# Performance work log

Measured on AMD Instinct MI355X. Metric: run time of the kernel, lower is better.

Reference implementation:

```python
import jax, jax.numpy as jnp
import numpy as np

C = 256
CI = C // 2  # inter_channel = 128
B, H, W = 8, 64, 64


def setup_inputs() -> dict:
    key = jax.random.key(0)
    ks = jax.random.split(key, 9)
    s = 0.02
    return {
        "x": jax.random.normal(ks[0], (B, C, H, W), jnp.float32),
        "w_phi": jax.random.normal(ks[1], (CI, C), jnp.float32) * s,
        "b_phi": jax.random.normal(ks[2], (CI,), jnp.float32) * s,
        "w_theta": jax.random.normal(ks[3], (CI, C), jnp.float32) * s,
        "b_theta": jax.random.normal(ks[4], (CI,), jnp.float32) * s,
        "w_g": jax.random.normal(ks[5], (CI, C), jnp.float32) * s,
        "b_g": jax.random.normal(ks[6], (CI,), jnp.float32) * s,
        "w_mask": jax.random.normal(ks[7], (C, CI), jnp.float32) * s,
        "b_mask": jax.random.normal(ks[8], (C,), jnp.float32) * s,
    }


def reference(x, w_phi, b_phi, w_theta, b_theta, w_g, b_g, w_mask, b_mask):
    b, c, h, w = x.shape
    n = h * w
    xf = x.reshape(b, c, n)  # [b, c, n]
    # 1x1 convs == per-position channel projections
    phi = jnp.einsum('dc,bcn->bdn', w_phi, xf) + b_phi[:, None]      # [b, ci, n]
    theta = jnp.einsum('dc,bcn->bnd', w_theta, xf) + b_theta[None, None, :]  # [b, n, ci]
    g = jnp.einsum('dc,bcn->bnd', w_g, xf) + b_g[None, None, :]      # [b, n, ci]
    # full self-attention over spatial positions (no scaling, as in source)
    scores = jnp.einsum('bnd,bdm->bnm', theta, phi)                  # [b, n, n]
    attn = jax.nn.softmax(scores, axis=-1)
    y = jnp.einsum('bnm,bmd->bnd', attn, g)                          # [b, n, ci]
    # mask conv (1x1) back to channel dim + residual
    mask = jnp.einsum('cd,bnd->bcn', w_mask, y) + b_mask[:, None]    # [b, c, n]
    return mask.reshape(b, c, h, w) + x
```

## Files before the change

### kernel.cpp

```cpp
#include <hip/hip_runtime.h>

#define BB 8
#define CC 256
#define DD 128
#define NN 4096

#define LOG2E 1.44269504f
#define MSHIFT 32.0f

typedef __attribute__((ext_vector_type(8))) short short8;
typedef __attribute__((ext_vector_type(4))) short short4v;
typedef __attribute__((ext_vector_type(4))) float f32x4;

static __device__ __forceinline__ unsigned short f2bf(float f) {
    unsigned u = __builtin_bit_cast(unsigned, f);
    u += 0x7FFFu + ((u >> 16) & 1u);
    return (unsigned short)(u >> 16);
}
static __device__ __forceinline__ unsigned short f2bf_trunc(float f) {
    return (unsigned short)(__builtin_bit_cast(unsigned, f) >> 16);
}
static __device__ __forceinline__ float bf2f(unsigned short h) {
    unsigned u = ((unsigned)h) << 16;
    return __builtin_bit_cast(float, u);
}
static __device__ __forceinline__ short8 pack8(float4 a, float4 b) {
    short8 r;
    r[0] = (short)f2bf(a.x); r[1] = (short)f2bf(a.y);
    r[2] = (short)f2bf(a.z); r[3] = (short)f2bf(a.w);
    r[4] = (short)f2bf(b.x); r[5] = (short)f2bf(b.y);
    r[6] = (short)f2bf(b.z); r[7] = (short)f2bf(b.w);
    return r;
}

__global__ __launch_bounds__(256) void k_transpose_x(
        const float* __restrict__ x, unsigned short* __restrict__ xT) {
    __shared__ __align__(16) unsigned short tile[64][66];
    int nb = blockIdx.x * 64, cb = blockIdx.y * 64, b = blockIdx.z;
    const float* xp = x + (size_t)b * CC * NN;
    int t = threadIdx.x;
#pragma unroll
    for (int i = 0; i < 2; i++) {
        int idx = t + 256 * i;
        int c_l = idx >> 3;
        int n0 = (idx & 7) * 8;
        const float* src = xp + (size_t)(cb + c_l) * NN + nb + n0;
        float4 v0 = *(const float4*)(src);
        float4 v1 = *(const float4*)(src + 4);
        tile[n0 + 0][c_l] = f2bf(v0.x);
        tile[n0 + 1][c_l] = f2bf(v0.y);
        tile[n0 + 2][c_l] = f2bf(v0.z);
        tile[n0 + 3][c_l] = f2bf(v0.w);
        tile[n0 + 4][c_l] = f2bf(v1.x);
        tile[n0 + 5][c_l] = f2bf(v1.y);
        tile[n0 + 6][c_l] = f2bf(v1.z);
        tile[n0 + 7][c_l] = f2bf(v1.w);
    }
    __syncthreads();
    unsigned short* xtp = xT + (size_t)b * NN * CC;
#pragma unroll
    for (int i = 0; i < 2; i++) {
        int idx = t + 256 * i;
        int n_l = idx >> 3;
        int c0 = (idx & 7) * 8;
        const unsigned int* row = (const unsigned int*)&tile[n_l][0];
        uint4 o;
        o.x = row[(c0 >> 1) + 0];
        o.y = row[(c0 >> 1) + 1];
        o.z = row[(c0 >> 1) + 2];
        o.w = row[(c0 >> 1) + 3];
        *(uint4*)(xtp + (size_t)(nb + n_l) * CC + cb + c0) = o;
    }
}

__global__ __launch_bounds__(256) void k_proj(
        const unsigned short* __restrict__ xT,
        const float* __restrict__ w_phi, const float* __restrict__ b_phi,
        const float* __restrict__ w_theta, const float* __restrict__ b_theta,
        const float* __restrict__ w_g, const float* __restrict__ b_g,
        unsigned short* __restrict__ qws, unsigned short* __restrict__ kws,
        unsigned short* __restrict__ vtws) {
    __shared__ __align__(16) unsigned short xs[128][72];
    __shared__ __align__(16) unsigned short rp[128][136];
    int nb = blockIdx.x * 128, proj = blockIdx.y, b = blockIdx.z;
    const float *W, *bias;
    if (proj == 0) { W = w_theta; bias = b_theta; }
    else if (proj == 1) { W = w_phi; bias = b_phi; }
    else { W = w_g; bias = b_g; }
    float scl = (proj == 0) ? LOG2E : 1.0f;
    int t = threadIdx.x, lane = t & 63, wave = t >> 6;
    int l16 = lane & 15, l4 = lane >> 4;

    f32x4 acc[2][8];
#pragma unroll
    for (int mf = 0; mf < 2; mf++)
#pragma unroll
        for (int nf = 0; nf < 8; nf++)
#pragma unroll
            for (int e = 0; e < 4; e++) acc[mf][nf][e] = 0.f;

    const unsigned short* xtp = xT + (size_t)b * NN * CC;
    for (int kc = 0; kc < 4; kc++) {
        int c0k = kc * 64;
        __syncthreads();
#pragma unroll
        for (int i = 0; i < 4; i++) {
            int idx = t + 256 * i;
            int n = idx >> 3, cc = (idx & 7) * 8;
            *(short8*)&xs[n][cc] = *(const short8*)(xtp + (size_t)(nb + n) * CC + c0k + cc);
        }
        __syncthreads();
        short8 af[2][2];
#pragma unroll
        for (int mf = 0; mf < 2; mf++)
#pragma unroll
            for (int ic = 0; ic < 2; ic++) {
                int d = wave * 32 + mf * 16 + l16;
                const float* wp = W + d * CC + c0k + ic * 32 + l4 * 8;
                af[mf][ic] = pack8(*(const float4*)wp, *(const float4*)(wp + 4));
            }
#pragma unroll
        for (int nf = 0; nf < 8; nf++)
#pragma unroll
            for (int ic = 0; ic < 2; ic++) {
                short8 bfr = *(const short8*)&xs[nf * 16 + l16][ic * 32 + l4 * 8];
                acc[0][nf] = __builtin_amdgcn_mfma_f32_16x16x32_bf16(af[0][ic], bfr, acc[0][nf], 0, 0, 0);
                acc[1][nf] = __builtin_amdgcn_mfma_f32_16x16x32_bf16(af[1][ic], bfr, acc[1][nf], 0, 0, 0);
            }
    }
    __syncthreads();
    if (proj < 2) {
        unsigned short* outp = (proj == 0 ? qws : kws) + (size_t)b * NN * DD;
#pragma unroll
        for (int mf = 0; mf < 2; mf++) {
            int d0 = wave * 32 + mf * 16 + l4 * 4;
            float bb[4];
#pragma unroll
            for (int r = 0; r < 4; r++) bb[r] = bias[d0 + r];
#pragma unroll
            for (int nf = 0; nf < 8; nf++) {
                short4v pk;
#pragma unroll
                for (int r = 0; r < 4; r++) pk[r] = (short)f2bf((acc[mf][nf][r] + bb[r]) * scl);
                *(short4v*)&rp[nf * 16 + l16][d0] = pk;
            }
        }
        __syncthreads();
#pragma unroll
        for (int i = 0; i < 8; i++) {
            int idx = t + 256 * i;
            int n = idx >> 4, dd = (idx & 15) * 8;
            *(short8*)(outp + (size_t)(nb + n) * DD + dd) = *(const short8*)&rp[n][dd];
        }
    } else {
#pragma unroll
        for (int mf = 0; mf < 2; mf++) {
            int drow = wave * 32 + mf * 16 + l4 * 4;
            float bb[4];
#pragma unroll
            for (int r = 0; r < 4; r++) bb[r] = bias[drow + r];
#pragma unroll
            for (int nf = 0; nf < 8; nf++)
#pragma unroll
                for (int r = 0; r < 4; r++)
                    rp[drow + r][nf * 16 + l16] = f2bf(acc[mf][nf][r] + bb[r]);
        }
        __syncthreads();
        unsigned short* outp = vtws + (size_t)b * DD * NN;
#pragma unroll
        for (int i = 0; i < 8; i++) {
            int idx = t + 256 * i;
            int d = idx >> 4, n0 = (idx & 15) * 8;
            *(short8*)(outp + (size_t)d * NN + nb + n0) = *(const short8*)&rp[d][n0];
        }
    }
}

__global__ __launch_bounds__(128, 4) void k_flash(
        const unsigned short* __restrict__ q, const unsigned short* __restrict__ kk,
        const unsigned short* __restrict__ vt, unsigned short* __restrict__ opart,
        float* __restrict__ lsums) {
    __shared__ __align__(16) unsigned short smem[12032];
    unsigned short (*Kt)[136] = (unsigned short (*)[136])smem;
    unsigned short (*Vt)[40]  = (unsigned short (*)[40])(smem + 4352);
    unsigned short (*Pt)[32][40] = (unsigned short (*)[32][40])(smem + 9472);

    int qb = blockIdx.x * 64, ks = blockIdx.y, b = blockIdx.z;
    int t = threadIdx.x, lane = t & 63, wave = t >> 6;
    int l16 = lane & 15, l4 = lane >> 4;
    const unsigned short* qp = q + (size_t)b * NN * DD;
    const unsigned short* kp = kk + (size_t)b * NN * DD;
    const unsigned short* vp = vt + (size_t)b * DD * NN;

    short8 qf[2][4];
#pragma unroll
    for (int m = 0; m < 2; m++) {
        int qrow = qb + wave * 32 + m * 16 + l16;
#pragma unroll
        for (int kc = 0; kc < 4; kc++)
            qf[m][kc] = *(const short8*)(qp + (size_t)qrow * DD + kc * 32 + l4 * 8);
    }

    f32x4 o[2][8];
    float lsum[2][4];
#pragma unroll
    for (int m = 0; m < 2; m++) {
#pragma unroll
        for (int df = 0; df < 8; df++)
#pragma unroll
            for (int e = 0; e < 4; e++) o[m][df][e] = 0.f;
#pragma unroll
        for (int r = 0; r < 4; r++) lsum[m][r] = 0.f;
    }

    int kbase = ks * (NN / 2);
    for (int it = 0; it < (NN / 2) / 32; ++it) {
        int mb = kbase + it * 32;
        __syncthreads();
#pragma unroll
        for (int i = 0; i < 4; i++) {
            int idx = t + 128 * i;
            int mr = idx >> 4, d0 = (idx & 15) * 8;
            *(short8*)&Kt[mr][d0] = *(const short8*)(kp + (size_t)(mb + mr) * DD + d0);
        }
#pragma unroll
        for (int i = 0; i < 4; i++) {
            int idx = t + 128 * i;
            int dr = idx >> 2, m0 = (idx & 3) * 8;
            *(short8*)&Vt[dr][m0] = *(const short8*)(vp + (size_t)dr * NN + mb + m0);
        }
        __syncthreads();

        f32x4 s[2][2];
#pragma unroll
        for (int m = 0; m < 2; m++)
#pragma unroll
            for (int nf = 0; nf < 2; nf++)
#pragma unroll
                for (int e = 0; e < 4; e++) s[m][nf][e] = -MSHIFT;
#pragma unroll
        for (int kc = 0; kc < 4; kc++)
#pragma unroll
            for (int nf = 0; nf < 2; nf++) {
                short8 bfr = *(const short8*)&Kt[nf * 16 + l16][kc * 32 + l4 * 8];
                s[0][nf] = __builtin_amdgcn_mfma_f32_16x16x32_bf16(qf[0][kc], bfr, s[0][nf], 0, 0, 0);
                s[1][nf] = __builtin_amdgcn_mfma_f32_16x16x32_bf16(qf[1][kc], bfr, s[1][nf], 0, 0, 0);
            }

#pragma unroll
        for (int m = 0; m < 2; m++)
#pragma unroll
            for (int nf = 0; nf < 2; nf++)
#pragma unroll
                for (int r = 0; r < 4; r++) {
                    float p = __builtin_exp2f(s[m][nf][r]);
                    lsum[m][r] += p;
                    Pt[wave][m * 16 + l4 * 4 + r][nf * 16 + l16] = f2bf_trunc(p);
                }
        asm volatile("s_waitcnt lgkmcnt(0)" ::: "memory");

        short8 pa0 = *(const short8*)&Pt[wave][l16][l4 * 8];
        short8 pa1 = *(const short8*)&Pt[wave][16 + l16][l4 * 8];
#pragma unroll
        for (int df = 0; df < 8; df++) {
            short8 vb = *(const short8*)&Vt[df * 16 + l16][l4 * 8];
            o[0][df] = __builtin_amdgcn_mfma_f32_16x16x32_bf16(pa0, vb, o[0][df], 0, 0, 0);
            o[1][df] = __builtin_amdgcn_mfma_f32_16x16x32_bf16(pa1, vb, o[1][df], 0, 0, 0);
        }
    }

    __syncthreads();
    unsigned short (*Ox)[136] = (unsigned short (*)[136])smem;
    float* Ls = (float*)((char*)smem + 17408);
    int rb = wave * 32;
#pragma unroll
    for (int m = 0; m < 2; m++) {
#pragma unroll
        for (int df = 0; df < 8; df++)
#pragma unroll
            for (int r = 0; r < 4; r++)
                Ox[rb + m * 16 + l4 * 4 + r][df * 16 + l16] = f2bf(o[m][df][r]);
#pragma unroll
        for (int r = 0; r < 4; r++) {
            float v = lsum[m][r];
            v += __shfl_xor(v, 1);
            v += __shfl_xor(v, 2);
            v += __shfl_xor(v, 4);
            v += __shfl_xor(v, 8);
            if (l16 == 0) Ls[rb + m * 16 + l4 * 4 + r] = v;
        }
    }
    __syncthreads();
    unsigned short* op = opart + (((size_t)ks * BB + b) * NN + qb) * DD;
#pragma unroll
    for (int i = 0; i < 8; i++) {
        int idx = t + 128 * i;
        int nr = idx >> 4, d0 = (idx & 15) * 8;
        *(short8*)(op + (size_t)nr * DD + d0) = *(const short8*)&Ox[nr][d0];
    }
    if (t < 64) lsums[((size_t)ks * BB + b) * NN + qb + t] = Ls[t];
}

__global__ __launch_bounds__(256) void k_maskout(
        const unsigned short* __restrict__ opart, const float* __restrict__ lsums,
        const float* __restrict__ w_mask, const float* __restrict__ b_mask,
        const float* __restrict__ x, float* __restrict__ out) {
    __shared__ __align__(16) unsigned short Ys[64][136];
    __shared__ float invl[64];
    int nb = blockIdx.x * 64, cs = blockIdx.y, b = blockIdx.z;
    int t = threadIdx.x, lane = t & 63, wave = t >> 6;
    int l16 = lane & 15, l4 = lane >> 4;

    const unsigned short* o0 = opart + ((size_t)b * NN + nb) * DD;
    const unsigned short* o1 = opart + (((size_t)BB + b) * NN + nb) * DD;
    if (t < 64) {
        float ls0 = lsums[(size_t)b * NN + nb + t];
        float ls1 = lsums[((size_t)BB + b) * NN + nb + t];
        invl[t] = 1.0f / (ls0 + ls1);
    }
    __syncthreads();
#pragma unroll
    for (int i = 0; i < 4; i++) {
        int idx = t + 256 * i;
        int nr = idx >> 4, d0 = (idx & 15) * 8;
        short8 a = *(const short8*)(o0 + (size_t)nr * DD + d0);
        short8 c = *(const short8*)(o1 + (size_t)nr * DD + d0);
        float inv = invl[nr];
        short8 yv;
#pragma unroll
        for (int j = 0; j < 8; j++)
            yv[j] = (short)f2bf((bf2f((unsigned short)a[j]) + bf2f((unsigned short)c[j])) * inv);
        *(short8*)&Ys[nr][d0] = yv;
    }
    __syncthreads();

    f32x4 acc[2][4];
#pragma unroll
    for (int mf = 0; mf < 2; mf++)
#pragma unroll
        for (int nf = 0; nf < 4; nf++)
#pragma unroll
            for (int e = 0; e < 4; e++) acc[mf][nf][e] = 0.f;

#pragma unroll
    for (int kc = 0; kc < 4; kc++) {
        int d0 = kc * 32 + l4 * 8;
        short8 af[2];
#pragma unroll
        for (int mf = 0; mf < 2; mf++) {
            int c = cs * 128 + wave * 32 + mf * 16 + l16;
            const float* wp = w_mask + c * DD + d0;
            af[mf] = pack8(*(const float4*)wp, *(const float4*)(wp + 4));
        }
#pragma unroll
        for (int nf = 0; nf < 4; nf++) {
            short8 bfr = *(const short8*)&Ys[nf * 16 + l16][d0];
#pragma unroll
            for (int mf = 0; mf < 2; mf++)
                acc[mf][nf] = __builtin_amdgcn_mfma_f32_16x16x32_bf16(af[mf], bfr, acc[mf][nf], 0, 0, 0);
        }
    }

    const float* xp = x + (size_t)b * CC * NN;
    float* op = out + (size_t)b * CC * NN;
#pragma unroll
    for (int mf = 0; mf < 2; mf++) {
        int c0 = cs * 128 + wave * 32 + mf * 16 + l4 * 4;
        float bb[4];
#pragma unroll
        for (int r = 0; r < 4; r++) bb[r] = b_mask[c0 + r];
#pragma unroll
        for (int r = 0; r < 4; r++) {
            size_t rowoff = (size_t)(c0 + r) * NN;
#pragma unroll
            for (int nf = 0; nf < 4; nf++) {
                int n = nb + nf * 16 + l16;
                op[rowoff + n] = acc[mf][nf][r] + bb[r] + xp[rowoff + n];
            }
        }
    }
}

extern "C" void kernel_launch(void* const* d_in, const int* in_sizes, int n_in,
                              void* d_out, int out_size, void* d_ws, size_t ws_size,
                              hipStream_t stream) {
    const float* x       = (const float*)d_in[0];
    const float* w_phi   = (const float*)d_in[1];
    const float* b_phi   = (const float*)d_in[2];
    const float* w_theta = (const float*)d_in[3];
    const float* b_theta = (const float*)d_in[4];
    const float* w_g     = (const float*)d_in[5];
    const float* b_g     = (const float*)d_in[6];
    const float* w_mask  = (const float*)d_in[7];
    const float* b_mask  = (const float*)d_in[8];
    float* out = (float*)d_out;

    char* ws = (char*)d_ws;
    unsigned short* xT    = (unsigned short*)(ws);
    unsigned short* opart = (unsigned short*)(ws);
    unsigned short* qw    = (unsigned short*)(ws + ((size_t)16 << 20));
    unsigned short* kw    = (unsigned short*)(ws + ((size_t)24 << 20));
    unsigned short* vtw   = (unsigned short*)(ws + ((size_t)32 << 20));
    float*          lsums = (float*)(ws + ((size_t)40 << 20));

    k_transpose_x<<<dim3(NN / 64, CC / 64, BB), 256, 0, stream>>>(x, xT);
    k_proj<<<dim3(NN / 128, 3, BB), 256, 0, stream>>>(xT, w_phi, b_phi, w_theta, b_theta,
                                                      w_g, b_g, qw, kw, vtw);
    k_flash<<<dim3(NN / 64, 2, BB), 128, 0, stream>>>(qw, kw, vtw, opart, lsums);
    k_maskout<<<dim3(NN / 64, 2, BB), 256, 0, stream>>>(opart, lsums, w_mask, b_mask, x, out);
}
```

Baseline: 270.3 us.

## Restructure flash attention kernel with 32x32 MFMA, larger tiles and register prefetch

Rewrites the attention kernel so each 512-thread block handles 256 query rows with 64-key tiles. Scores are computed as K·Q^T using 32x32x16 bf16 MFMA, so the probability fragments can be turned into the next MFMA's A operand in registers via cvt_pk_bf16 and permlane32 swaps, removing the LDS round trip for P. K/V tiles are stored in XOR-swizzled shared memory, the next tile is prefetched into registers while the current one computes, and block IDs are remapped to spread batches across XCDs. In exchange, register pressure rises and shared memory per block grows, which may reduce occupancy.

```diff
diff --git a/kernel.cpp b/kernel.cpp
--- a/kernel.cpp
+++ b/kernel.cpp
@@ -11,14 +11,13 @@
 typedef __attribute__((ext_vector_type(8))) short short8;
 typedef __attribute__((ext_vector_type(4))) short short4v;
 typedef __attribute__((ext_vector_type(4))) float f32x4;
+typedef __attribute__((ext_vector_type(16))) float f32x16;
+typedef __attribute__((ext_vector_type(4))) unsigned int u32x4;
 
 static __device__ __forceinline__ unsigned short f2bf(float f) {
     unsigned u = __builtin_bit_cast(unsigned, f);
     u += 0x7FFFu + ((u >> 16) & 1u);
     return (unsigned short)(u >> 16);
-}
-static __device__ __forceinline__ unsigned short f2bf_trunc(float f) {
-    return (unsigned short)(__builtin_bit_cast(unsigned, f) >> 16);
 }
 static __device__ __forceinline__ float bf2f(unsigned short h) {
     unsigned u = ((unsigned)h) << 16;
@@ -31,6 +30,19 @@
     r[4] = (short)f2bf(b.x); r[5] = (short)f2bf(b.y);
     r[6] = (short)f2bf(b.z); r[7] = (short)f2bf(b.w);
     return r;
+}
+static __device__ __forceinline__ unsigned cvtpk_bf16(float lo, float hi) {
+    unsigned r;
+    asm("v_cvt_pk_bf16_f32 %0, %1, %2" : "=v"(r) : "v"(lo), "v"(hi));
+    return r;
+}
+static __device__ __forceinline__ void pl32swap(unsigned &a, unsigned &b) {
+#if __has_builtin(__builtin_amdgcn_permlane32_swap)
+    auto r = __builtin_amdgcn_permlane32_swap((int)a, (int)b, false, false);
+    a = (unsigned)r[0]; b = (unsigned)r[1];
+#else
+    asm("v_permlane32_swap_b32 %0, %1" : "+v"(a), "+v"(b));
+#endif
 }
 
 __global__ __launch_bounds__(256) void k_transpose_x(
@@ -176,129 +188,178 @@
     }
 }
 
-__global__ __launch_bounds__(128, 4) void k_flash(
+__global__ __launch_bounds__(512, 2) void k_flash(
         const unsigned short* __restrict__ q, const unsigned short* __restrict__ kk,
         const unsigned short* __restrict__ vt, unsigned short* __restrict__ opart,
         float* __restrict__ lsums) {
-    __shared__ __align__(16) unsigned short smem[12032];
-    unsigned short (*Kt)[136] = (unsigned short (*)[136])smem;
-    unsigned short (*Vt)[40]  = (unsigned short (*)[40])(smem + 4352);
-    unsigned short (*Pt)[32][40] = (unsigned short (*)[32][40])(smem + 9472);
-
-    int qb = blockIdx.x * 64, ks = blockIdx.y, b = blockIdx.z;
+    __shared__ __align__(16) unsigned char smem[49152];
+    unsigned short* Ksm = (unsigned short*)smem;
+    unsigned short* Vsm = (unsigned short*)(smem + 32768);
+
+    int bid = blockIdx.x + 16 * (blockIdx.y + 2 * blockIdx.z);
+    int lb = (bid & 7) * 32 + (bid >> 3);
+    int qt = lb & 15;
+    int ks = (lb >> 4) & 1;
+    int b  = lb >> 5;
+    int qb = qt * 256;
+
     int t = threadIdx.x, lane = t & 63, wave = t >> 6;
-    int l16 = lane & 15, l4 = lane >> 4;
-    const unsigned short* qp = q + (size_t)b * NN * DD;
+    int l31 = lane & 31, hi = lane >> 5;
+
+    const unsigned short* qp = q  + (size_t)b * NN * DD;
     const unsigned short* kp = kk + (size_t)b * NN * DD;
     const unsigned short* vp = vt + (size_t)b * DD * NN;
 
-    short8 qf[2][4];
-#pragma unroll
-    for (int m = 0; m < 2; m++) {
-        int qrow = qb + wave * 32 + m * 16 + l16;
-#pragma unroll
-        for (int kc = 0; kc < 4; kc++)
-            qf[m][kc] = *(const short8*)(qp + (size_t)qrow * DD + kc * 32 + l4 * 8);
-    }
-
-    f32x4 o[2][8];
-    float lsum[2][4];
-#pragma unroll
-    for (int m = 0; m < 2; m++) {
-#pragma unroll
-        for (int df = 0; df < 8; df++)
-#pragma unroll
-            for (int e = 0; e < 4; e++) o[m][df][e] = 0.f;
-#pragma unroll
-        for (int r = 0; r < 4; r++) lsum[m][r] = 0.f;
-    }
+    short8 qreg[8];
+    {
+        int qrow = qb + wave * 32 + l31;
+#pragma unroll
+        for (int kc = 0; kc < 8; kc++)
+            qreg[kc] = *(const short8*)(qp + (size_t)qrow * DD + kc * 16 + hi * 8);
+    }
+
+    f32x16 o[4];
+#pragma unroll
+    for (int df = 0; df < 4; df++)
+#pragma unroll
+        for (int e = 0; e < 16; e++) o[df][e] = 0.f;
+    float lsum = 0.f;
 
     int kbase = ks * (NN / 2);
-    for (int it = 0; it < (NN / 2) / 32; ++it) {
-        int mb = kbase + it * 32;
+    const int NIT = (NN / 2) / 64;
+
+    {
+        uint4 k0[2], v0[2];
+#pragma unroll
+        for (int i = 0; i < 2; i++) {
+            int idx = t + 512 * i;
+            k0[i] = *(const uint4*)(kp + (size_t)(kbase + (idx >> 4)) * DD + (idx & 15) * 8);
+            v0[i] = *(const uint4*)(vp + (size_t)(idx >> 3) * NN + kbase + (idx & 7) * 8);
+        }
+#pragma unroll
+        for (int i = 0; i < 2; i++) {
+            int idx = t + 512 * i;
+            int rk = idx >> 4, ck = idx & 15;
+            *(uint4*)((char*)Ksm + rk * 256 + ((ck ^ (rk & 7)) << 4)) = k0[i];
+            int rv = idx >> 3, cv = idx & 7;
+            *(uint4*)((char*)Vsm + rv * 128 + ((cv ^ (rv & 7)) << 4)) = v0[i];
+        }
+    }
+    __syncthreads();
+
+    for (int it = 0; it < NIT; ++it) {
+        uint4 kreg[2], vreg[2];
+        bool pf = (it + 1 < NIT);
+        if (pf) {
+            int mb2 = kbase + (it + 1) * 64;
+#pragma unroll
+            for (int i = 0; i < 2; i++) {
+                int idx = t + 512 * i;
+                kreg[i] = *(const uint4*)(kp + (size_t)(mb2 + (idx >> 4)) * DD + (idx & 15) * 8);
+            }
+#pragma unroll
+            for (int i = 0; i < 2; i++) {
+                int idx = t + 512 * i;
+                vreg[i] = *(const uint4*)(vp + (size_t)(idx >> 3) * NN + mb2 + (idx & 7) * 8);
+            }
+        }
+
+        f32x16 sa[2];
+#pragma unroll
+        for (int mf = 0; mf < 2; mf++)
+#pragma unroll
+            for (int e = 0; e < 16; e++) sa[mf][e] = -MSHIFT;
+#pragma unroll
+        for (int kc = 0; kc < 8; kc++) {
+#pragma unroll
+            for (int mf = 0; mf < 2; mf++) {
+                int row = mf * 32 + l31;
+                short8 a = *(const short8*)((const char*)Ksm + row * 256 +
+                                            ((((kc << 1) | hi) ^ (row & 7)) << 4));
+                sa[mf] = __builtin_amdgcn_mfma_f32_32x32x16_bf16(a, qreg[kc], sa[mf], 0, 0, 0);
+            }
+        }
+
+        u32x4 pa[4];
+#pragma unroll
+        for (int mf = 0; mf < 2; mf++) {
+            float p[16];
+#pragma unroll
+            for (int r = 0; r < 16; r++) {
+                p[r] = __builtin_exp2f(sa[mf][r]);
+                lsum += p[r];
+            }
+#pragma unroll
+            for (int h = 0; h < 2; h++) {
+                unsigned a0 = cvtpk_bf16(p[8 * h + 0], p[8 * h + 1]);
+                unsigned a1 = cvtpk_bf16(p[8 * h + 2], p[8 * h + 3]);
+                unsigned b0 = cvtpk_bf16(p[8 * h + 4], p[8 * h + 5]);
+                unsigned b1 = cvtpk_bf16(p[8 * h + 6], p[8 * h + 7]);
+                pl32swap(a0, b0);
+                pl32swap(a1, b1);
+                u32x4 v; v[0] = a0; v[1] = a1; v[2] = b0; v[3] = b1;
+                pa[mf * 2 + h] = v;
+            }
+        }
+
+#pragma unroll
+        for (int df = 0; df < 4; df++) {
+            int row = df * 32 + l31;
+#pragma unroll
+            for (int c = 0; c < 4; c++) {
+                short8 bfr = *(const short8*)((const char*)Vsm + row * 128 +
+                                              ((((c << 1) | hi) ^ (row & 7)) << 4));
+                o[df] = __builtin_amdgcn_mfma_f32_32x32x16_bf16(
+                    __builtin_bit_cast(short8, pa[c]), bfr, o[df], 0, 0, 0);
+            }
+        }
+
+        __syncthreads();
+        if (pf) {
+#pragma unroll
+            for (int i = 0; i < 2; i++) {
+                int idx = t + 512 * i;
+                int rk = idx >> 4, ck = idx & 15;
+                *(uint4*)((char*)Ksm + rk * 256 + ((ck ^ (rk & 7)) << 4)) = kreg[i];
+            }
+#pragma unroll
+            for (int i = 0; i < 2; i++) {
+                int idx = t + 512 * i;
+                int rv = idx >> 3, cv = idx & 7;
+                *(uint4*)((char*)Vsm + rv * 128 + ((cv ^ (rv & 7)) << 4)) = vreg[i];
+            }
+        }
+        __syncthreads();
+    }
+
+    {
+        float tot = lsum + __shfl_xor(lsum, 32);
+        if (lane < 32)
+            lsums[((size_t)ks * BB + b) * NN + qb + wave * 32 + l31] = tot;
+    }
+    unsigned short (*Ox)[136] = (unsigned short (*)[136])smem;
+    unsigned short* op = opart + (((size_t)ks * BB + b) * NN + qb) * DD;
+#pragma unroll
+    for (int half = 0; half < 2; half++) {
+        if ((wave >> 2) == half) {
+            int rb = (wave & 3) * 32;
+#pragma unroll
+            for (int df = 0; df < 4; df++)
+#pragma unroll
+                for (int r = 0; r < 16; r++) {
+                    int qr = (r & 3) + 8 * (r >> 2) + 4 * hi;
+                    Ox[rb + qr][df * 32 + l31] = f2bf(o[df][r]);
+                }
+        }
         __syncthreads();
 #pragma unroll
         for (int i = 0; i < 4; i++) {
-            int idx = t + 128 * i;
-            int mr = idx >> 4, d0 = (idx & 15) * 8;
-            *(short8*)&Kt[mr][d0] = *(const short8*)(kp + (size_t)(mb + mr) * DD + d0);
-        }
-#pragma unroll
-        for (int i = 0; i < 4; i++) {
-            int idx = t + 128 * i;
-            int dr = idx >> 2, m0 = (idx & 3) * 8;
-            *(short8*)&Vt[dr][m0] = *(const short8*)(vp + (size_t)dr * NN + mb + m0);
-        }
-        __syncthreads();
-
-        f32x4 s[2][2];
-#pragma unroll
-        for (int m = 0; m < 2; m++)
-#pragma unroll
-            for (int nf = 0; nf < 2; nf++)
-#pragma unroll
-                for (int e = 0; e < 4; e++) s[m][nf][e] = -MSHIFT;
-#pragma unroll
-        for (int kc = 0; kc < 4; kc++)
-#pragma unroll
-            for (int nf = 0; nf < 2; nf++) {
-                short8 bfr = *(const short8*)&Kt[nf * 16 + l16][kc * 32 + l4 * 8];
-                s[0][nf] = __builtin_amdgcn_mfma_f32_16x16x32_bf16(qf[0][kc], bfr, s[0][nf], 0, 0, 0);
-                s[1][nf] = __builtin_amdgcn_mfma_f32_16x16x32_bf16(qf[1][kc], bfr, s[1][nf], 0, 0, 0);
-            }
-
-#pragma unroll
-        for (int m = 0; m < 2; m++)
-#pragma unroll
-            for (int nf = 0; nf < 2; nf++)
-#pragma unroll
-                for (int r = 0; r < 4; r++) {
-                    float p = __builtin_exp2f(s[m][nf][r]);
-                    lsum[m][r] += p;
-                    Pt[wave][m * 16 + l4 * 4 + r][nf * 16 + l16] = f2bf_trunc(p);
-                }
-        asm volatile("s_waitcnt lgkmcnt(0)" ::: "memory");
-
-        short8 pa0 = *(const short8*)&Pt[wave][l16][l4 * 8];
-        short8 pa1 = *(const short8*)&Pt[wave][16 + l16][l4 * 8];
-#pragma unroll
-        for (int df = 0; df < 8; df++) {
-            short8 vb = *(const short8*)&Vt[df * 16 + l16][l4 * 8];
-            o[0][df] = __builtin_amdgcn_mfma_f32_16x16x32_bf16(pa0, vb, o[0][df], 0, 0, 0);
-            o[1][df] = __builtin_amdgcn_mfma_f32_16x16x32_bf16(pa1, vb, o[1][df], 0, 0, 0);
-        }
-    }
-
-    __syncthreads();
-    unsigned short (*Ox)[136] = (unsigned short (*)[136])smem;
-    float* Ls = (float*)((char*)smem + 17408);
-    int rb = wave * 32;
-#pragma unroll
-    for (int m = 0; m < 2; m++) {
-#pragma unroll
-        for (int df = 0; df < 8; df++)
-#pragma unroll
-            for (int r = 0; r < 4; r++)
-                Ox[rb + m * 16 + l4 * 4 + r][df * 16 + l16] = f2bf(o[m][df][r]);
-#pragma unroll
-        for (int r = 0; r < 4; r++) {
-            float v = lsum[m][r];
-            v += __shfl_xor(v, 1);
-            v += __shfl_xor(v, 2);
-            v += __shfl_xor(v, 4);
-            v += __shfl_xor(v, 8);
-            if (l16 == 0) Ls[rb + m * 16 + l4 * 4 + r] = v;
-        }
-    }
-    __syncthreads();
-    unsigned short* op = opart + (((size_t)ks * BB + b) * NN + qb) * DD;
-#pragma unroll
-    for (int i = 0; i < 8; i++) {
-        int idx = t + 128 * i;
-        int nr = idx >> 4, d0 = (idx & 15) * 8;
-        *(short8*)(op + (size_t)nr * DD + d0) = *(const short8*)&Ox[nr][d0];
-    }
-    if (t < 64) lsums[((size_t)ks * BB + b) * NN + qb + t] = Ls[t];
+            int idx = t + 512 * i;
+            int rr = idx >> 4, c0 = (idx & 15) * 8;
+            *(short8*)(op + (size_t)(half * 128 + rr) * DD + c0) = *(const short8*)&Ox[rr][c0];
+        }
+        __syncthreads();
+    }
 }
 
 __global__ __launch_bounds__(256) void k_maskout(
@@ -406,6 +467,6 @@
     k_transpose_x<<<dim3(NN / 64, CC / 64, BB), 256, 0, stream>>>(x, xT);
     k_proj<<<dim3(NN / 128, 3, BB), 256, 0, stream>>>(xT, w_phi, b_phi, w_theta, b_theta,
                                                       w_g, b_g, qw, kw, vtw);
-    k_flash<<<dim3(NN / 64, 2, BB), 128, 0, stream>>>(qw, kw, vtw, opart, lsums);
+    k_flash<<<dim3(NN / 256, 2, BB), 512, 0, stream>>>(qw, kw, vtw, opart, lsums);
     k_maskout<<<dim3(NN / 64, 2, BB), 256, 0, stream>>>(opart, lsums, w_mask, b_mask, x, out);
 }
```

Result: slower. 289.7 us (+7.2%).
